# Performance work log

Measured on AMD Instinct MI355X. Metric: run time of the kernel, lower is better.

The kernel has to match this reference:

```python
import jax, jax.numpy as jnp
import numpy as np

L, H, NH, NKV, HD, S, P, FF = 2, 2048, 16, 2, 128, 1024, 1024, 5632
G = NH // NKV
THETA = 1000000.0
EPS = 1e-6
SCALE = 1.0 / np.sqrt(HD).astype(np.float32)


def rms_norm(x, w):
    return x * jax.lax.rsqrt(jnp.mean(x * x, axis=-1, keepdims=True) + EPS) * w


def rotate_half(x):
    x1, x2 = jnp.split(x, 2, axis=-1)
    return jnp.concatenate([-x2, x1], axis=-1)


def setup_inputs() -> dict:
    key = jax.random.key(0)
    ks = iter(jax.random.split(key, 16))
    w = lambda shape: jax.random.normal(next(ks), shape, jnp.float32) * 0.02
    return {
        'inputs_embeds': jax.random.normal(next(ks), (1, S, H), jnp.float32),
        'position_ids': (jnp.arange(S, dtype=jnp.int32) + P)[None, :],
        'past_k': jax.random.normal(next(ks), (L, 1, NKV, P, HD), jnp.float32),
        'past_v': jax.random.normal(next(ks), (L, 1, NKV, P, HD), jnp.float32),
        'ln1_w': jnp.ones((L, H), jnp.float32),
        'wq': w((L, H, NH * HD)), 'bq': jnp.zeros((L, NH * HD), jnp.float32),
        'wk': w((L, H, NKV * HD)), 'bk': jnp.zeros((L, NKV * HD), jnp.float32),
        'wv': w((L, H, NKV * HD)), 'bv': jnp.zeros((L, NKV * HD), jnp.float32),
        'wo': w((L, NH * HD, H)),
        'ln2_w': jnp.ones((L, H), jnp.float32),
        'w_gate': w((L, H, FF)), 'w_up': w((L, H, FF)), 'w_down': w((L, FF, H)),
        'norm_w': jnp.ones((H,), jnp.float32),
    }


def reference(inputs_embeds, position_ids, past_k, past_v, ln1_w, wq, bq, wk, bk,
              wv, bv, wo, ln2_w, w_gate, w_up, w_down, norm_w):
    pos = position_ids.astype(jnp.float32)                      # [1,S]
    inv_freq = 1.0 / (THETA ** (jnp.arange(0, HD, 2, dtype=jnp.float32) / HD))
    freqs = pos[:, :, None] * inv_freq                          # [1,S,HD/2]
    emb = jnp.concatenate([freqs, freqs], axis=-1)              # [1,S,HD]
    cos = jnp.cos(emb)[:, None]                                 # [1,1,S,HD]
    sin = jnp.sin(emb)[:, None]
    T = P + S
    k_pos = jnp.arange(T, dtype=jnp.float32)
    # causal mask over absolute positions: future keys masked with -65504
    mask = jnp.where(k_pos[None, None, None, :] > pos[:, None, :, None],
                     jnp.float32(-65504.0), jnp.float32(0.0))   # [1,1,S,T]

    hidden = inputs_embeds
    present = []
    for i in range(L):
        residual = hidden
        h = rms_norm(hidden, ln1_w[i])
        q = (h @ wq[i] + bq[i]).reshape(1, S, NH, HD).transpose(0, 2, 1, 3)
        k = (h @ wk[i] + bk[i]).reshape(1, S, NKV, HD).transpose(0, 2, 1, 3)
        v = (h @ wv[i] + bv[i]).reshape(1, S, NKV, HD).transpose(0, 2, 1, 3)
        q = q * cos + rotate_half(q) * sin
        k = k * cos + rotate_half(k) * sin
        k = jnp.concatenate([past_k[i], k], axis=2)             # [1,NKV,T,HD]
        v = jnp.concatenate([past_v[i], v], axis=2)
        present.append(k)
        present.append(v)
        # GQA: group query heads per kv head instead of expanding k/v
        qg = q.reshape(1, NKV, G, S, HD)
        attn = jnp.einsum('bkgsd,bktd->bkgst', qg, k) * SCALE   # [1,NKV,G,S,T]
        attn = jax.nn.softmax(attn + mask[:, :, None], axis=-1)
        out = jnp.einsum('bkgst,bktd->bkgsd', attn, v)
        out = out.reshape(1, NH, S, HD).transpose(0, 2, 1, 3).reshape(1, S, H)
        hidden = residual + out @ wo[i]
        residual = hidden
        h = rms_norm(hidden, ln2_w[i])
        h = (jax.nn.silu(h @ w_gate[i]) * (h @ w_up[i])) @ w_down[i]
        hidden = residual + h
    hidden = rms_norm(hidden, norm_w)
    return (hidden, *present)
```

## Files before the change

kernel.cpp:

```cpp
#include <hip/hip_runtime.h>

#define L_ 2
#define H_ 2048
#define NH_ 16
#define NKV_ 2
#define HD_ 128
#define S_ 1024
#define P_ 1024
#define T_ 2048
#define FF_ 5632
#define QKVN_ 2560
#define KOFF_ 2048
#define VOFF_ 2304

#define EPS_ 1e-6f
#define SCALE_ 0.08838834764831845f
#define DEFER_THR_ 8.0f

typedef __bf16 bf16_t;
typedef unsigned int u32;
typedef __bf16 bx8 __attribute__((ext_vector_type(8)));
typedef __bf16 bx4 __attribute__((ext_vector_type(4)));
typedef float  fx4 __attribute__((ext_vector_type(4)));

__device__ __forceinline__ fx4 mfma16(bx8 a, bx8 b, fx4 c) {
  return __builtin_amdgcn_mfma_f32_16x16x32_bf16(a, b, c, 0, 0, 0);
}

#define GLL16(gsrc, ldst) __builtin_amdgcn_global_load_lds( \
    (__attribute__((address_space(1))) void*)(gsrc),        \
    (__attribute__((address_space(3))) void*)(ldst), 16, 0, 0)

__device__ __forceinline__ bx8 lds_read_b128(char* p) {
  u32 a = (u32)(uintptr_t)(__attribute__((address_space(3))) void*)p;
  bx8 d;
  asm volatile("ds_read_b128 %0, %1" : "=v"(d) : "v"(a));
  return d;
}

__device__ __forceinline__ int xcd_swizzle(int orig, int nwg) {
  int q = nwg >> 3, r = nwg & 7;
  int xcd = orig & 7, lid = orig >> 3;
  return (xcd < r ? xcd * (q + 1) : r * (q + 1) + (xcd - r) * q) + lid;
}

__global__ void k_rope_tables(const int* __restrict__ pos, float* __restrict__ ct, float* __restrict__ st) {
  int i = blockIdx.x * 256 + threadIdx.x;
  if (i >= S_ * 64) return;
  int s = i >> 6, d = i & 63;
  float p = (float)pos[s];
  float inv = expf(-(float)(2 * d) * (13.815510557964274f / 128.0f));
  float f = p * inv;
  ct[i] = cosf(f);
  st[i] = sinf(f);
}

__global__ void k_copy4(const float* __restrict__ in, float* __restrict__ out, int n4) {
  int i = blockIdx.x * 256 + threadIdx.x;
  if (i < n4) ((fx4*)out)[i] = ((const fx4*)in)[i];
}

__global__ void k_cbias(const float* __restrict__ bq, const float* __restrict__ bk,
                        const float* __restrict__ bv, float* __restrict__ cb) {
  int i = blockIdx.x * 256 + threadIdx.x;
  if (i >= L_ * QKVN_) return;
  int l = i / QKVN_, j = i % QKVN_;
  float v;
  if (j < KOFF_)      v = bq[l * KOFF_ + j];
  else if (j < VOFF_) v = bk[l * (NKV_ * HD_) + j - KOFF_];
  else                v = bv[l * (NKV_ * HD_) + j - VOFF_];
  cb[i] = v;
}

template<int OUTBF>
__global__ __launch_bounds__(256) void k_rmsnorm(const float* __restrict__ x, const float* __restrict__ w,
                                                 void* __restrict__ y) {
  int row = blockIdx.x, tid = threadIdx.x;
  const fx4* xr = (const fx4*)(x + (size_t)row * H_);
  fx4 v0 = xr[tid], v1 = xr[tid + 256];
  float ss = v0[0]*v0[0] + v0[1]*v0[1] + v0[2]*v0[2] + v0[3]*v0[3]
           + v1[0]*v1[0] + v1[1]*v1[1] + v1[2]*v1[2] + v1[3]*v1[3];
  #pragma unroll
  for (int off = 32; off > 0; off >>= 1) ss += __shfl_xor(ss, off);
  __shared__ float red[4];
  if ((tid & 63) == 0) red[tid >> 6] = ss;
  __syncthreads();
  float tot = red[0] + red[1] + red[2] + red[3];
  float rs = rsqrtf(tot * (1.0f / H_) + EPS_);
  const fx4* wr_ = (const fx4*)w;
  fx4 w0 = wr_[tid], w1 = wr_[tid + 256];
  if (OUTBF) {
    bf16_t* yb = (bf16_t*)y + (size_t)row * H_;
    bx4 o0, o1;
    #pragma unroll
    for (int i = 0; i < 4; i++) { o0[i] = (bf16_t)(v0[i] * rs * w0[i]); o1[i] = (bf16_t)(v1[i] * rs * w1[i]); }
    *(bx4*)&yb[tid * 4] = o0;
    *(bx4*)&yb[(tid + 256) * 4] = o1;
  } else {
    float* yf = (float*)y + (size_t)row * H_;
    fx4 o0, o1;
    #pragma unroll
    for (int i = 0; i < 4; i++) { o0[i] = v0[i] * rs * w0[i]; o1[i] = v1[i] * rs * w1[i]; }
    *(fx4*)&yf[tid * 4] = o0;
    *(fx4*)&yf[(tid + 256) * 4] = o1;
  }
}

__global__ __launch_bounds__(256) void k_transpose_w(const float* __restrict__ in, bf16_t* __restrict__ out,
                                                     int R, int C) {
  __shared__ __attribute__((aligned(16))) float Tt[64 * 68];
  int tid = threadIdx.x;
  int c0 = blockIdx.x * 64, r0 = blockIdx.y * 64;
  #pragma unroll
  for (int j = 0; j < 4; j++) {
    int c = j * 256 + tid;
    int row = c >> 4, col = (c & 15) * 4;
    *(fx4*)&Tt[row * 68 + col] = *(const fx4*)&in[(size_t)(r0 + row) * C + c0 + col];
  }
  __syncthreads();
  #pragma unroll
  for (int j = 0; j < 2; j++) {
    int c = j * 256 + tid;
    int n = c >> 3, ko = (c & 7) * 8;
    bx8 o;
    #pragma unroll
    for (int i = 0; i < 8; i++) o[i] = (bf16_t)Tt[(ko + i) * 68 + n];
    *(bx8*)&out[(size_t)(c0 + n) * R + r0 + ko] = o;
  }
}

template<int OUTBF, int HASB, int HASR>
__global__ __launch_bounds__(256) void k_gemm(const bf16_t* __restrict__ A, const bf16_t* __restrict__ Bt,
                                              const float* __restrict__ bias, const float* __restrict__ res,
                                              void* __restrict__ out, int M, int N, int K, int gy) {
  __shared__ __attribute__((aligned(16))) bf16_t sA[3][64 * 64];
  __shared__ __attribute__((aligned(16))) bf16_t sB[3][128 * 64];
  int tid = threadIdx.x;
  int w = tid >> 6, lane = tid & 63, g = lane >> 4, r = lane & 15;
  int wr = w >> 1, wc = w & 1;
  int swzid = xcd_swizzle((int)blockIdx.x, (int)gridDim.x);
  int m0 = (swzid % gy) * 64;
  int n0 = (swzid / gy) * 128;
  fx4 acc[2][4] = {};
  int swz = (r & 7) << 4;
  int col0 = (g * 16) ^ swz;
  int col1 = (64 + g * 16) ^ swz;
  int wbase = (tid & ~63) * 16;
  int nk = K >> 6;

  auto STAGE = [&](int buf, int k0) {
    #pragma unroll
    for (int j = 0; j < 2; j++) {
      int d = (j * 256 + tid) * 16;
      int row = d >> 7;
      int inrow = (d & 127) ^ ((row & 7) << 4);
      GLL16((const char*)(A + (size_t)(m0 + row) * K + k0) + inrow,
            (char*)&sA[buf][0] + j * 4096 + wbase);
    }
    #pragma unroll
    for (int j = 0; j < 4; j++) {
      int d = (j * 256 + tid) * 16;
      int row = d >> 7;
      int inrow = (d & 127) ^ ((row & 7) << 4);
      GLL16((const char*)(Bt + (size_t)(n0 + row) * K + k0) + inrow,
            (char*)&sB[buf][0] + j * 4096 + wbase);
    }
  };

  STAGE(0, 0);
  STAGE(1, 64);
  asm volatile("s_waitcnt vmcnt(6)" ::: "memory");
  __builtin_amdgcn_s_barrier();
  __builtin_amdgcn_sched_barrier(0);
  int cur = 0;
  for (int t = 0; t < nk; t++) {
    if (t + 2 < nk) STAGE((cur + 2) % 3, (t + 2) << 6);
    char* pa = (char*)&sA[cur][0] + (wr * 32 + r) * 128;
    char* pb = (char*)&sB[cur][0] + (wc * 64 + r) * 128;
    bx8 fa[2][2], fb[4][2];
    #pragma unroll
    for (int m = 0; m < 2; m++) {
      fa[m][0] = lds_read_b128(pa + m * 2048 + col0);
      fa[m][1] = lds_read_b128(pa + m * 2048 + col1);
    }
    #pragma unroll
    for (int n = 0; n < 4; n++) {
      fb[n][0] = lds_read_b128(pb + n * 2048 + col0);
      fb[n][1] = lds_read_b128(pb + n * 2048 + col1);
    }
    asm volatile("s_waitcnt lgkmcnt(0)" ::: "memory");
    __builtin_amdgcn_sched_barrier(0);
    #pragma unroll
    for (int kk = 0; kk < 2; kk++)
      #pragma unroll
      for (int n = 0; n < 4; n++) {
        acc[0][n] = mfma16(fa[0][kk], fb[n][kk], acc[0][n]);
        acc[1][n] = mfma16(fa[1][kk], fb[n][kk], acc[1][n]);
      }
    if (t + 1 < nk) {
      if (t + 2 < nk) { asm volatile("s_waitcnt vmcnt(6)" ::: "memory"); }
      else            { asm volatile("s_waitcnt vmcnt(0)" ::: "memory"); }
      __builtin_amdgcn_s_barrier();
      __builtin_amdgcn_sched_barrier(0);
    }
    cur = (cur + 1) % 3;
  }
  #pragma unroll
  for (int m = 0; m < 2; m++)
    #pragma unroll
    for (int n = 0; n < 4; n++) {
      int col = n0 + wc * 64 + n * 16 + r;
      #pragma unroll
      for (int rr = 0; rr < 4; rr++) {
        int row = m0 + wr * 32 + m * 16 + 4 * g + rr;
        float v = acc[m][n][rr];
        if (HASB) v += bias[col];
        if (HASR) v += res[(size_t)row * N + col];
        if (OUTBF) ((bf16_t*)out)[(size_t)row * N + col] = (bf16_t)v;
        else       ((float*)out)[(size_t)row * N + col] = v;
      }
    }
}

__global__ void k_rope_q(const bf16_t* __restrict__ qkv, const float* __restrict__ ct,
                         const float* __restrict__ st, bf16_t* __restrict__ qout) {
  int i = blockIdx.x * 256 + threadIdx.x;
  if (i >= S_ * NH_ * 64) return;
  int d = i & 63, h = (i >> 6) & 15, s = i >> 10;
  size_t ib = (size_t)s * QKVN_ + h * HD_;
  float x1 = (float)qkv[ib + d];
  float x2 = (float)qkv[ib + d + 64];
  float c = ct[s * 64 + d], sn = st[s * 64 + d];
  size_t ob = ((size_t)h * S_ + s) * HD_;
  qout[ob + d]      = (bf16_t)(x1 * c - x2 * sn);
  qout[ob + d + 64] = (bf16_t)(x2 * c + x1 * sn);
}

__global__ void k_build_k(const bf16_t* __restrict__ qkv, const float* __restrict__ pastk,
                          const float* __restrict__ ct, const float* __restrict__ st,
                          bf16_t* __restrict__ kc, float* __restrict__ pk_out) {
  int i = blockIdx.x * 256 + threadIdx.x;
  if (i >= NKV_ * T_ * 64) return;
  int d = i & 63, t = (i >> 6) & (T_ - 1), kv = i >> 17;
  size_t cb = ((size_t)kv * T_ + t) * HD_;
  if (t < P_) {
    size_t pb = ((size_t)kv * P_ + t) * HD_;
    float a = pastk[pb + d], b = pastk[pb + d + 64];
    kc[cb + d] = (bf16_t)a; kc[cb + d + 64] = (bf16_t)b;
    pk_out[cb + d] = a;     pk_out[cb + d + 64] = b;
  } else {
    int s = t - P_;
    size_t ib = (size_t)s * QKVN_ + KOFF_ + kv * HD_;
    float x1 = (float)qkv[ib + d];
    float x2 = (float)qkv[ib + d + 64];
    float c = ct[s * 64 + d], sn = st[s * 64 + d];
    float k1 = x1 * c - x2 * sn, k2 = x2 * c + x1 * sn;
    kc[cb + d] = (bf16_t)k1; kc[cb + d + 64] = (bf16_t)k2;
    pk_out[cb + d] = k1;     pk_out[cb + d + 64] = k2;
  }
}

__global__ __launch_bounds__(256) void k_build_vt(const bf16_t* __restrict__ qkv, const float* __restrict__ pastv,
                                                  bf16_t* __restrict__ vt, float* __restrict__ pv_out) {
  int t0 = blockIdx.x * 64, d0 = blockIdx.y * 64, kv = blockIdx.z;
  __shared__ __attribute__((aligned(16))) float Tt[64 * 68];
  int tid = threadIdx.x;
  if (t0 < P_) {
    #pragma unroll
    for (int j = 0; j < 4; j++) {
      int c = j * 256 + tid;
      int row = c >> 4, col = (c & 15) * 4;
      int t = t0 + row;
      fx4 v = *(const fx4*)&pastv[((size_t)kv * P_ + t) * HD_ + d0 + col];
      *(fx4*)&Tt[row * 68 + col] = v;
      *(fx4*)&pv_out[((size_t)kv * T_ + t) * HD_ + d0 + col] = v;
    }
  } else {
    #pragma unroll
    for (int j = 0; j < 4; j++) {
      int c = j * 256 + tid;
      int row = c >> 4, col = (c & 15) * 4;
      int t = t0 + row;
      bx4 b = *(const bx4*)&qkv[(size_t)(t - P_) * QKVN_ + VOFF_ + kv * HD_ + d0 + col];
      fx4 v;
      #pragma unroll
      for (int q = 0; q < 4; q++) v[q] = (float)b[q];
      *(fx4*)&Tt[row * 68 + col] = v;
      *(fx4*)&pv_out[((size_t)kv * T_ + t) * HD_ + d0 + col] = v;
    }
  }
  __syncthreads();
  #pragma unroll
  for (int j = 0; j < 2; j++) {
    int c = j * 256 + tid;
    int n = c >> 3, ko = (c & 7) * 8;
    bx8 o;
    #pragma unroll
    for (int i = 0; i < 8; i++) o[i] = (bf16_t)Tt[(ko + i) * 68 + n];
    *(bx8*)&vt[((size_t)kv * HD_ + d0 + n) * T_ + t0 + ko] = o;
  }
}

__global__ __launch_bounds__(256) void k_attn(const bf16_t* __restrict__ Q, const bf16_t* __restrict__ Kc,
                                              const bf16_t* __restrict__ VT, bf16_t* __restrict__ O) {
  __shared__ __attribute__((aligned(16))) bf16_t Klds[2][64 * 128];
  __shared__ __attribute__((aligned(16))) bf16_t Vlds[2][128 * 64];
  __shared__ __attribute__((aligned(16))) bf16_t Plds[4][16][72];
  int tid = threadIdx.x;
  int w = tid >> 6, lane = tid & 63, g = lane >> 4, r = lane & 15;
  int h = blockIdx.y, kv = h >> 3;
  int m0 = blockIdx.x * 64;
  int qr0 = m0 + w * 16;
  const bf16_t* qb = Q + ((size_t)h * S_ + qr0 + r) * HD_ + g * 8;
  bx8 qf[4];
  #pragma unroll
  for (int kc = 0; kc < 4; kc++) qf[kc] = *(const bx8*)(qb + kc * 32);
  fx4 of[8] = {};
  float mrun[4], lrun[4];
  #pragma unroll
  for (int i = 0; i < 4; i++) { mrun[i] = -1e30f; lrun[i] = 0.0f; }
  int lim = P_ + qr0 + 4 * g;
  int ntile = (P_ + m0 + 64) >> 6;
  const char* kg = (const char*)(Kc + (size_t)kv * T_ * HD_);
  const char* vg = (const char*)(VT + (size_t)kv * HD_ * T_);
  int wbase = (tid & ~63) * 16;

  auto STAGE = [&](int buf, int t0) {
    #pragma unroll
    for (int j = 0; j < 4; j++) {
      int D = j * 4096 + tid * 16;
      int row = D >> 8, inrow = D & 255;
      const char* src = kg + (size_t)(t0 + row) * 256 + (inrow ^ ((row & 7) << 4));
      GLL16(src, (char*)&Klds[buf][0] + j * 4096 + wbase);
    }
    #pragma unroll
    for (int j = 0; j < 4; j++) {
      int D = j * 4096 + tid * 16;
      int row = D >> 7, inrow = D & 127;
      const char* src = vg + (size_t)row * 4096 + (size_t)t0 * 2 + (inrow ^ ((row & 7) << 4));
      GLL16(src, (char*)&Vlds[buf][0] + j * 4096 + wbase);
    }
  };

  STAGE(0, 0);
  __syncthreads();
  int cur = 0;
  for (int t = 0; t < ntile; t++) {
    int t0 = t * 64;
    if (t + 1 < ntile) STAGE(cur ^ 1, t0 + 64);
    const char* kb = (const char*)&Klds[cur][0];
    fx4 sc[4] = {};
    #pragma unroll
    for (int nt = 0; nt < 4; nt++) {
      int row = nt * 16 + r;
      const char* kr = kb + row * 256;
      int sz = (row & 7) << 4;
      #pragma unroll
      for (int kc = 0; kc < 4; kc++)
        sc[nt] = mfma16(qf[kc], *(const bx8*)(kr + (((kc * 32 + g * 8) * 2) ^ sz)), sc[nt]);
    }
    float lm[4] = {-1e30f, -1e30f, -1e30f, -1e30f};
    #pragma unroll
    for (int nt = 0; nt < 4; nt++)
      #pragma unroll
      for (int rr = 0; rr < 4; rr++) {
        int key = t0 + nt * 16 + r;
        float sv = sc[nt][rr] * SCALE_;
        sv = (key > lim + rr) ? -1e30f : sv;
        sc[nt][rr] = sv;
        lm[rr] = fmaxf(lm[rr], sv);
      }
    int ok = (lm[0] <= mrun[0] + DEFER_THR_) & (lm[1] <= mrun[1] + DEFER_THR_) &
             (lm[2] <= mrun[2] + DEFER_THR_) & (lm[3] <= mrun[3] + DEFER_THR_);
    if (!__all(ok)) {
      float av[4];
      #pragma unroll
      for (int off = 1; off < 16; off <<= 1)
        #pragma unroll
        for (int rr = 0; rr < 4; rr++) lm[rr] = fmaxf(lm[rr], __shfl_xor(lm[rr], off));
      #pragma unroll
      for (int rr = 0; rr < 4; rr++) {
        float mn = fmaxf(mrun[rr], lm[rr]);
        av[rr] = __expf(mrun[rr] - mn);
        mrun[rr] = mn;
        lrun[rr] *= av[rr];
      }
      #pragma unroll
      for (int f = 0; f < 8; f++)
        #pragma unroll
        for (int rr = 0; rr < 4; rr++) of[f][rr] *= av[rr];
    }
    #pragma unroll
    for (int nt = 0; nt < 4; nt++)
      #pragma unroll
      for (int rr = 0; rr < 4; rr++) {
        float pr = __expf(sc[nt][rr] - mrun[rr]);
        lrun[rr] += pr;
        Plds[w][4 * g + rr][nt * 16 + r] = (bf16_t)pr;
      }
    asm volatile("s_waitcnt lgkmcnt(0)" ::: "memory");
    __builtin_amdgcn_sched_barrier(0);
    const char* vb = (const char*)&Vlds[cur][0];
    #pragma unroll
    for (int ks = 0; ks < 2; ks++) {
      bx8 pa = *(const bx8*)&Plds[w][r][ks * 32 + g * 8];
      #pragma unroll
      for (int dt = 0; dt < 8; dt++) {
        int row = dt * 16 + r;
        of[dt] = mfma16(pa, *(const bx8*)(vb + row * 128 + (((ks * 32 + g * 8) * 2) ^ ((row & 7) << 4))), of[dt]);
      }
    }
    __syncthreads();
    cur ^= 1;
  }
  #pragma unroll
  for (int off = 1; off < 16; off <<= 1)
    #pragma unroll
    for (int rr = 0; rr < 4; rr++) lrun[rr] += __shfl_xor(lrun[rr], off);
  float li[4];
  #pragma unroll
  for (int rr = 0; rr < 4; rr++) li[rr] = 1.0f / lrun[rr];
  #pragma unroll
  for (int dt = 0; dt < 8; dt++)
    #pragma unroll
    for (int rr = 0; rr < 4; rr++)
      O[(size_t)(qr0 + 4 * g + rr) * H_ + h * HD_ + dt * 16 + r] = (bf16_t)(of[dt][rr] * li[rr]);
}

__global__ void k_silu_mul(const bf16_t* __restrict__ gb, const bf16_t* __restrict__ ub,
                           bf16_t* __restrict__ ob, int n8) {
  int i = blockIdx.x * 256 + threadIdx.x;
  if (i >= n8) return;
  bx8 gv = ((const bx8*)gb)[i], uv = ((const bx8*)ub)[i];
  bx8 ov;
  #pragma unroll
  for (int j = 0; j < 8; j++) {
    float x = (float)gv[j], y = (float)uv[j];
    float s = x / (1.0f + __expf(-x));
    ov[j] = (bf16_t)(s * y);
  }
  ((bx8*)ob)[i] = ov;
}

extern "C" void kernel_launch(void* const* d_in, const int* in_sizes, int n_in,
                              void* d_out, int out_size, void* d_ws, size_t ws_size,
                              hipStream_t stream) {
  const float* embeds = (const float*)d_in[0];
  const int*   pos    = (const int*)d_in[1];
  const float* past_k = (const float*)d_in[2];
  const float* past_v = (const float*)d_in[3];
  const float* ln1    = (const float*)d_in[4];
  const float* wq     = (const float*)d_in[5];
  const float* bq     = (const float*)d_in[6];
  const float* wk     = (const float*)d_in[7];
  const float* bk     = (const float*)d_in[8];
  const float* wv     = (const float*)d_in[9];
  const float* bv     = (const float*)d_in[10];
  const float* wo     = (const float*)d_in[11];
  const float* ln2    = (const float*)d_in[12];
  const float* wg     = (const float*)d_in[13];
  const float* wu     = (const float*)d_in[14];
  const float* wd     = (const float*)d_in[15];
  const float* normw  = (const float*)d_in[16];

  char* wsp = (char*)d_ws;
  auto take = [&](size_t n) { char* p = wsp; wsp += (n + 255) & ~(size_t)255; return (void*)p; };
  float*  cos_t  = (float*)take((size_t)S_ * 64 * 4);
  float*  sin_t  = (float*)take((size_t)S_ * 64 * 4);
  float*  cbias  = (float*)take((size_t)L_ * QKVN_ * 4);
  float*  hidden = (float*)take((size_t)S_ * H_ * 4);
  bf16_t* hnorm  = (bf16_t*)take((size_t)S_ * H_ * 2);
  bf16_t* qkv    = (bf16_t*)take((size_t)S_ * QKVN_ * 2);
  bf16_t* qrope  = (bf16_t*)take((size_t)NH_ * S_ * HD_ * 2);
  bf16_t* kcache = (bf16_t*)take((size_t)NKV_ * T_ * HD_ * 2);
  bf16_t* vtr    = (bf16_t*)take((size_t)NKV_ * HD_ * T_ * 2);
  bf16_t* attno  = (bf16_t*)take((size_t)S_ * H_ * 2);
  bf16_t* gateb  = (bf16_t*)take((size_t)S_ * FF_ * 2);
  bf16_t* upb    = (bf16_t*)take((size_t)S_ * FF_ * 2);
  bf16_t* hgb    = (bf16_t*)take((size_t)S_ * FF_ * 2);
  bf16_t* wT     = (bf16_t*)take((size_t)FF_ * H_ * 2);

  float* out_h = (float*)d_out;

  k_rope_tables<<<256, 256, 0, stream>>>(pos, cos_t, sin_t);
  k_cbias<<<(L_ * QKVN_ + 255) / 256, 256, 0, stream>>>(bq, bk, bv, cbias);
  k_copy4<<<(S_ * H_ / 4 + 255) / 256, 256, 0, stream>>>(embeds, hidden, S_ * H_ / 4);

  for (int l = 0; l < L_; l++) {
    const float* wq_l = wq + (size_t)l * H_ * (NH_ * HD_);
    const float* wk_l = wk + (size_t)l * H_ * (NKV_ * HD_);
    const float* wv_l = wv + (size_t)l * H_ * (NKV_ * HD_);
    const float* wo_l = wo + (size_t)l * (NH_ * HD_) * H_;
    const float* wg_l = wg + (size_t)l * H_ * FF_;
    const float* wu_l = wu + (size_t)l * H_ * FF_;
    const float* wd_l = wd + (size_t)l * FF_ * H_;
    const float* pk_in = past_k + (size_t)l * NKV_ * P_ * HD_;
    const float* pv_in = past_v + (size_t)l * NKV_ * P_ * HD_;
    float* pk_out = out_h + (size_t)S_ * H_ + (size_t)l * 2 * NKV_ * T_ * HD_;
    float* pv_out = pk_out + (size_t)NKV_ * T_ * HD_;

    k_rmsnorm<1><<<S_, 256, 0, stream>>>(hidden, ln1 + (size_t)l * H_, hnorm);
    k_transpose_w<<<dim3(32, 32), 256, 0, stream>>>(wq_l, wT, H_, NH_ * HD_);
    k_transpose_w<<<dim3(4, 32), 256, 0, stream>>>(wk_l, wT + (size_t)KOFF_ * H_, H_, NKV_ * HD_);
    k_transpose_w<<<dim3(4, 32), 256, 0, stream>>>(wv_l, wT + (size_t)VOFF_ * H_, H_, NKV_ * HD_);
    k_gemm<1, 1, 0><<<(QKVN_ / 128) * (S_ / 64), 256, 0, stream>>>(
        hnorm, wT, cbias + (size_t)l * QKVN_, nullptr, qkv, S_, QKVN_, H_, S_ / 64);
    k_rope_q<<<(S_ * NH_ * 64) / 256, 256, 0, stream>>>(qkv, cos_t, sin_t, qrope);
    k_build_k<<<(NKV_ * T_ * 64) / 256, 256, 0, stream>>>(qkv, pk_in, cos_t, sin_t, kcache, pk_out);
    k_build_vt<<<dim3(T_ / 64, HD_ / 64, NKV_), 256, 0, stream>>>(qkv, pv_in, vtr, pv_out);
    k_attn<<<dim3(S_ / 64, NH_), 256, 0, stream>>>(qrope, kcache, vtr, attno);
    k_transpose_w<<<dim3(32, 32), 256, 0, stream>>>(wo_l, wT, NH_ * HD_, H_);
    k_gemm<0, 0, 1><<<(H_ / 128) * (S_ / 64), 256, 0, stream>>>(
        attno, wT, nullptr, hidden, hidden, S_, H_, NH_ * HD_, S_ / 64);
    k_rmsnorm<1><<<S_, 256, 0, stream>>>(hidden, ln2 + (size_t)l * H_, hnorm);
    k_transpose_w<<<dim3(88, 32), 256, 0, stream>>>(wg_l, wT, H_, FF_);
    k_gemm<1, 0, 0><<<(FF_ / 128) * (S_ / 64), 256, 0, stream>>>(
        hnorm, wT, nullptr, nullptr, gateb, S_, FF_, H_, S_ / 64);
    k_transpose_w<<<dim3(88, 32), 256, 0, stream>>>(wu_l, wT, H_, FF_);
    k_gemm<1, 0, 0><<<(FF_ / 128) * (S_ / 64), 256, 0, stream>>>(
        hnorm, wT, nullptr, nullptr, upb, S_, FF_, H_, S_ / 64);
    k_silu_mul<<<(S_ * FF_ / 8) / 256, 256, 0, stream>>>(gateb, upb, hgb, S_ * FF_ / 8);
    k_transpose_w<<<dim3(32, 88), 256, 0, stream>>>(wd_l, wT, FF_, H_);
    k_gemm<0, 0, 1><<<(H_ / 128) * (S_ / 64), 256, 0, stream>>>(
        hgb, wT, nullptr, hidden, hidden, S_, H_, FF_, S_ / 64);
  }
  k_rmsnorm<0><<<S_, 256, 0, stream>>>(hidden, normw, out_h);
}
```

Measured before the change: 601.7 us.

## Replace attention loop syncthreads with explicit vmcnt waits and batched LDS reads

In the flash-attention loop, __syncthreads is replaced with raw s_barrier plus explicit vmcnt waits, so the prefetch of the next K/V tile can stay in flight while only the current tile's loads are awaited. K and V fragment reads become batched inline-asm ds_read_b128 issued ahead of their MFMAs, separated by lgkmcnt waits and sched barriers, and P writes use ds_write_b16. The goal is to drop full memory drains at barriers and group LDS latency. The hand-counted vmcnt(8) and the removed end-of-iteration sync carry a correctness risk, and holding K/V fragments in registers raises register pressure.

```diff
diff --git a/kernel.cpp b/kernel.cpp
--- a/kernel.cpp
+++ b/kernel.cpp
@@ -36,6 +36,12 @@
   bx8 d;
   asm volatile("ds_read_b128 %0, %1" : "=v"(d) : "v"(a));
   return d;
+}
+__device__ __forceinline__ void lds_write_b16(char* p, float v) {
+  u32 a = (u32)(uintptr_t)(__attribute__((address_space(3))) void*)p;
+  bf16_t b = (bf16_t)v;
+  u32 d = (u32)__builtin_bit_cast(unsigned short, b);
+  asm volatile("ds_write_b16 %0, %1" :: "v"(a), "v"(d));
 }
 
 __device__ __forceinline__ int xcd_swizzle(int orig, int nwg) {
@@ -343,22 +349,40 @@
   };
 
   STAGE(0, 0);
-  __syncthreads();
+  asm volatile("s_waitcnt vmcnt(0)" ::: "memory");
+  __builtin_amdgcn_s_barrier();
+  __builtin_amdgcn_sched_barrier(0);
   int cur = 0;
   for (int t = 0; t < ntile; t++) {
     int t0 = t * 64;
-    if (t + 1 < ntile) STAGE(cur ^ 1, t0 + 64);
-    const char* kb = (const char*)&Klds[cur][0];
-    fx4 sc[4] = {};
+    int pref = (t + 1 < ntile);
+    if (pref) {
+      STAGE(cur ^ 1, t0 + 64);
+      asm volatile("s_waitcnt vmcnt(8)" ::: "memory");
+    } else {
+      asm volatile("s_waitcnt vmcnt(0)" ::: "memory");
+    }
+    __builtin_amdgcn_s_barrier();
+    __builtin_amdgcn_sched_barrier(0);
+    char* kb = (char*)&Klds[cur][0];
+    bx8 kf[4][4];
     #pragma unroll
     for (int nt = 0; nt < 4; nt++) {
       int row = nt * 16 + r;
-      const char* kr = kb + row * 256;
+      char* kr = kb + row * 256;
       int sz = (row & 7) << 4;
       #pragma unroll
       for (int kc = 0; kc < 4; kc++)
-        sc[nt] = mfma16(qf[kc], *(const bx8*)(kr + (((kc * 32 + g * 8) * 2) ^ sz)), sc[nt]);
-    }
+        kf[nt][kc] = lds_read_b128(kr + (((kc * 32 + g * 8) * 2) ^ sz));
+    }
+    asm volatile("s_waitcnt lgkmcnt(0)" ::: "memory");
+    __builtin_amdgcn_sched_barrier(0);
+    fx4 sc[4] = {};
+    #pragma unroll
+    for (int nt = 0; nt < 4; nt++)
+      #pragma unroll
+      for (int kc = 0; kc < 4; kc++)
+        sc[nt] = mfma16(qf[kc], kf[nt][kc], sc[nt]);
     float lm[4] = {-1e30f, -1e30f, -1e30f, -1e30f};
     #pragma unroll
     for (int nt = 0; nt < 4; nt++)
@@ -396,21 +420,27 @@
       for (int rr = 0; rr < 4; rr++) {
         float pr = __expf(sc[nt][rr] - mrun[rr]);
         lrun[rr] += pr;
-        Plds[w][4 * g + rr][nt * 16 + r] = (bf16_t)pr;
+        lds_write_b16((char*)&Plds[w][4 * g + rr][nt * 16 + r], pr);
       }
     asm volatile("s_waitcnt lgkmcnt(0)" ::: "memory");
     __builtin_amdgcn_sched_barrier(0);
-    const char* vb = (const char*)&Vlds[cur][0];
+    char* vb = (char*)&Vlds[cur][0];
     #pragma unroll
     for (int ks = 0; ks < 2; ks++) {
-      bx8 pa = *(const bx8*)&Plds[w][r][ks * 32 + g * 8];
+      bx8 pa = lds_read_b128((char*)&Plds[w][r][ks * 32 + g * 8]);
+      bx8 vf[8];
       #pragma unroll
       for (int dt = 0; dt < 8; dt++) {
         int row = dt * 16 + r;
-        of[dt] = mfma16(pa, *(const bx8*)(vb + row * 128 + (((ks * 32 + g * 8) * 2) ^ ((row & 7) << 4))), of[dt]);
+        vf[dt] = lds_read_b128(vb + row * 128 + (((ks * 32 + g * 8) * 2) ^ ((row & 7) << 4)));
       }
-    }
-    __syncthreads();
+      asm volatile("s_waitcnt lgkmcnt(0)" ::: "memory");
+      __builtin_amdgcn_sched_barrier(0);
+      #pragma unroll
+      for (int dt = 0; dt < 8; dt++)
+        of[dt] = mfma16(pa, vf[dt], of[dt]);
+    }
+    __builtin_amdgcn_s_barrier();
     cur ^= 1;
   }
   #pragma unroll
```

New measurement: 588.3 us. -2.2%, faster.
